# Performance work log

Hardware: AMD Instinct MI355X
Metric: run time of the kernel (lower is better)

The kernel has to match this reference:

```python
import jax, jax.numpy as jnp
import numpy as np

N_NODES = 100000
N_EDGES = 3200000
D_IN = 16
D_OUT = 32


def setup_inputs() -> dict:
    key = jax.random.key(0)
    ks = jax.random.split(key, 8)
    x = jax.random.normal(ks[0], (N_NODES, D_IN), dtype=jnp.float32)
    edge_index = jax.random.randint(ks[1], (2, N_EDGES), 0, N_NODES, dtype=jnp.int64)
    s = 1.0 / np.sqrt(D_IN)
    # mlp1: Linear(16,16) -> ReLU -> Linear(16,16)
    w1 = jax.random.uniform(ks[2], (D_IN, D_IN), jnp.float32, -s, s)
    b1 = jax.random.uniform(ks[3], (D_IN,), jnp.float32, -s, s)
    w2 = jax.random.uniform(ks[4], (D_IN, D_IN), jnp.float32, -s, s)
    b2 = jax.random.uniform(ks[5], (D_IN,), jnp.float32, -s, s)
    # SAGEConv(16,32): lin_l (neighbors, with bias), lin_r (root, no bias)
    wl = jax.random.uniform(ks[6], (D_IN, D_OUT), jnp.float32, -s, s)
    bl = jnp.zeros((D_OUT,), jnp.float32)
    wr = jax.random.uniform(ks[7], (D_IN, D_OUT), jnp.float32, -s, s)
    return {"x": x, "edge_index": edge_index, "w1": w1, "b1": b1,
            "w2": w2, "b2": b2, "wl": wl, "bl": bl, "wr": wr}


def reference(x, edge_index, w1, b1, w2, b2, wl, bl, wr):
    # MLP: Linear -> ReLU -> Linear
    h = jax.nn.relu(x @ w1 + b1) @ w2 + b2  # [N, 16]
    src, dst = edge_index[0], edge_index[1]
    # mean aggregation of neighbor (source) features at destination nodes
    msg = h[src]  # [E, 16]
    summed = jax.ops.segment_sum(msg, dst, num_segments=N_NODES)  # [N, 16]
    cnt = jax.ops.segment_sum(jnp.ones((msg.shape[0],), h.dtype), dst,
                              num_segments=N_NODES)
    mean = summed / jnp.maximum(cnt, 1.0)[:, None]
    # SAGEConv: lin_l(aggr) + lin_r(root)
    out = mean @ wl + bl + h @ wr  # [N, 32]
    return out
```

## Files before the change

kernel.cpp:

```cpp
#include <hip/hip_runtime.h>

#define D_IN_C 16
#define D_OUT_C 32
#define NB_LOG 6
#define NB (1 << NB_LOG)
#define NB_MASK (NB - 1)
#define MAXBUCK 1600
#define EPB 12800

__global__ __launch_bounds__(256) void mlp_kernel(
    const float* __restrict__ x,
    const float* __restrict__ w1, const float* __restrict__ b1,
    const float* __restrict__ w2, const float* __restrict__ b2,
    float* __restrict__ h, float* __restrict__ summed, int* __restrict__ cnt,
    int* __restrict__ gcount, int nbuck, int n_nodes) {
  __shared__ float sw1[256];
  __shared__ float sw2[256];
  __shared__ float sb1[16];
  __shared__ float sb2[16];
  int t = threadIdx.x;
  sw1[t] = w1[t];
  sw2[t] = w2[t];
  if (t < 16) { sb1[t] = b1[t]; sb2[t] = b2[t]; }
  __syncthreads();

  int n = blockIdx.x * blockDim.x + t;

  if (gcount && n < nbuck) gcount[n] = 0;
  if (n >= n_nodes) return;

  float xi[16];
  const float4* xr = (const float4*)(x + (size_t)n * 16);
  float4 v0 = xr[0], v1 = xr[1], v2 = xr[2], v3 = xr[3];
  xi[0]=v0.x; xi[1]=v0.y; xi[2]=v0.z; xi[3]=v0.w;
  xi[4]=v1.x; xi[5]=v1.y; xi[6]=v1.z; xi[7]=v1.w;
  xi[8]=v2.x; xi[9]=v2.y; xi[10]=v2.z; xi[11]=v2.w;
  xi[12]=v3.x; xi[13]=v3.y; xi[14]=v3.z; xi[15]=v3.w;

  float t1[16];
#pragma unroll
  for (int j = 0; j < 16; ++j) {
    float acc = sb1[j];
#pragma unroll
    for (int k = 0; k < 16; ++k) acc += xi[k] * sw1[k * 16 + j];
    t1[j] = fmaxf(acc, 0.0f);
  }
  float hh[16];
#pragma unroll
  for (int j = 0; j < 16; ++j) {
    float acc = sb2[j];
#pragma unroll
    for (int k = 0; k < 16; ++k) acc += t1[k] * sw2[k * 16 + j];
    hh[j] = acc;
  }

  float4* hw = (float4*)(h + (size_t)n * 16);
  hw[0] = make_float4(hh[0], hh[1], hh[2], hh[3]);
  hw[1] = make_float4(hh[4], hh[5], hh[6], hh[7]);
  hw[2] = make_float4(hh[8], hh[9], hh[10], hh[11]);
  hw[3] = make_float4(hh[12], hh[13], hh[14], hh[15]);

  if (cnt) cnt[n] = 0;
  if (summed) {
    float4* sz = (float4*)(summed + (size_t)n * 16);
    float4 z = make_float4(0.f, 0.f, 0.f, 0.f);
    sz[0] = z; sz[1] = z; sz[2] = z; sz[3] = z;
  }
}

__global__ __launch_bounds__(1024) void hist_kernel(
    const int* __restrict__ dst, int* __restrict__ gcount,
    int nbuck, int n_edges) {
  __shared__ int lcnt[MAXBUCK];
  int t = threadIdx.x;
  for (int i = t; i < MAXBUCK; i += 1024) lcnt[i] = 0;
  __syncthreads();
  int e0 = blockIdx.x * EPB;
  int e1 = e0 + EPB; if (e1 > n_edges) e1 = n_edges;
  for (int e = e0 + t; e < e1; e += 1024)
    atomicAdd(&lcnt[dst[e] >> NB_LOG], 1);
  __syncthreads();
  for (int b = t; b < nbuck; b += 1024) {
    int c = lcnt[b];
    if (c) atomicAdd(&gcount[b], c);
  }
}

__global__ __launch_bounds__(256) void scan_kernel(
    const int* __restrict__ gcount, int* __restrict__ base,
    int* __restrict__ cursor, int nbuck) {
  __shared__ int ps[256];
  int t = threadIdx.x;
  int per = (nbuck + 255) / 256;
  int beg = t * per;
  int end = beg + per; if (end > nbuck) end = nbuck;
  int sum = 0;
  for (int i = beg; i < end; ++i) sum += gcount[i];
  ps[t] = sum;
  __syncthreads();
#pragma unroll
  for (int off = 1; off < 256; off <<= 1) {
    int add = (t >= off) ? ps[t - off] : 0;
    __syncthreads();
    ps[t] += add;
    __syncthreads();
  }
  int run = ps[t] - sum;
  for (int i = beg; i < end; ++i) {
    base[i] = run;
    cursor[i] = run;
    run += gcount[i];
  }
  if (t == 255) base[nbuck] = ps[255];
}

__global__ __launch_bounds__(1024) void bin_kernel(
    const int* __restrict__ src, const int* __restrict__ dst,
    int* __restrict__ cursor, unsigned int* __restrict__ ebuf,
    int nbuck, int n_edges) {
  __shared__ int lcnt[MAXBUCK];
  __shared__ int lspan[MAXBUCK];
  int t = threadIdx.x;
  for (int i = t; i < MAXBUCK; i += 1024) lcnt[i] = 0;
  __syncthreads();
  int e0 = blockIdx.x * EPB;
  int e1 = e0 + EPB; if (e1 > n_edges) e1 = n_edges;
  for (int e = e0 + t; e < e1; e += 1024)
    atomicAdd(&lcnt[dst[e] >> NB_LOG], 1);
  __syncthreads();
  for (int b = t; b < nbuck; b += 1024) {
    int c = lcnt[b];
    lspan[b] = c ? atomicAdd(&cursor[b], c) : 0;
    lcnt[b] = 0;
  }
  __syncthreads();
  for (int e = e0 + t; e < e1; e += 1024) {
    int d = dst[e];
    int b = d >> NB_LOG;
    int r = atomicAdd(&lcnt[b], 1);
    ebuf[lspan[b] + r] =
        ((unsigned int)src[e] << NB_LOG) | (unsigned int)(d & NB_MASK);
  }
}

__global__ __launch_bounds__(256) void agg_out_kernel(
    const float* __restrict__ h, const unsigned int* __restrict__ ebuf,
    const int* __restrict__ base,
    const float* __restrict__ wl, const float* __restrict__ bl,
    const float* __restrict__ wr, float* __restrict__ out, int n_nodes) {
  __shared__ float ssum[NB * 16];
  __shared__ int   scnt[NB];
  __shared__ float stg[4 * 8 * 64];
  __shared__ float swl[512];
  __shared__ float swr[512];
  __shared__ float sbl[32];

  int t = threadIdx.x;
  int b = blockIdx.x;

  for (int i = t; i < 512; i += 256) { swl[i] = wl[i]; swr[i] = wr[i]; }
  if (t < 32) sbl[t] = bl[t];
#pragma unroll
  for (int i = t; i < NB * 16; i += 256) ssum[i] = 0.0f;
  if (t < NB) scnt[t] = 0;
  __syncthreads();

  int beg = base[b];
  int end = base[b + 1];

  int wid  = t >> 6;
  int lane = t & 63;
  int cl   = lane >> 4;
  int k    = lane & 15;

  const char* hb = (const char*)h;
  float* stgw = &stg[wid * 512];

  for (int pb = beg + wid * 32; pb < end; pb += 128) {
    unsigned int e[8];
#pragma unroll
    for (int u = 0; u < 8; ++u) {
      int idx = pb + 4 * u + cl;
      int cidx = idx < end ? idx : end - 1;
      e[u] = ebuf[cidx];
    }
#pragma unroll
    for (int u = 0; u < 8; ++u) {
      const void* gp = (const void*)(hb + ((e[u] & ~63u) + (unsigned)(k << 2)));
      __builtin_amdgcn_global_load_lds(
          (const __attribute__((address_space(1))) void*)gp,
          (__attribute__((address_space(3))) void*)&stgw[u * 64], 4, 0, 0);
    }
    asm volatile("s_waitcnt vmcnt(0)" ::: "memory");
#pragma unroll
    for (int u = 0; u < 8; ++u) {
      int idx = pb + 4 * u + cl;
      if (idx < end) {
        float v = stgw[u * 64 + lane];
        int dl = (int)(e[u] & NB_MASK);
        atomicAdd(&ssum[dl * 16 + k], v);
        if (k == 0) atomicAdd(&scnt[dl], 1);
      }
    }
  }
  __syncthreads();

  int j = t & 31;
  for (int nl = t >> 5; nl < NB; nl += 8) {
    int n = b * NB + nl;
    if (n >= n_nodes) break;
    float inv = 1.0f / fmaxf((float)scnt[nl], 1.0f);
    float acc = sbl[j];
    const float* hr = h + (size_t)n * 16;
#pragma unroll
    for (int kk = 0; kk < 16; ++kk) {
      float mv = ssum[nl * 16 + kk] * inv;
      acc += mv * swl[kk * 32 + j] + hr[kk] * swr[kk * 32 + j];
    }
    out[(size_t)n * 32 + j] = acc;
  }
}

__global__ __launch_bounds__(256) void scatter_kernel(
    const int* __restrict__ src, const int* __restrict__ dst,
    const float* __restrict__ h, float* __restrict__ summed,
    int* __restrict__ cnt, long long n_edges) {
  long long tid = (long long)blockIdx.x * blockDim.x + threadIdx.x;
  long long e = tid >> 4;
  int k = (int)(tid & 15);
  if (e >= n_edges) return;
  int s = src[e];
  int d = dst[e];
  float val = h[(size_t)s * 16 + k];
  atomicAdd(&summed[(size_t)d * 16 + k], val);
  if (k == 0) atomicAdd(&cnt[d], 1);
}

__global__ __launch_bounds__(256) void out_kernel(
    const float* __restrict__ h, const float* __restrict__ summed,
    const int* __restrict__ cnt,
    const float* __restrict__ wl, const float* __restrict__ bl,
    const float* __restrict__ wr, float* __restrict__ out, int n_nodes) {
  __shared__ float swl[512];
  __shared__ float swr[512];
  __shared__ float sbl[32];
  int t = threadIdx.x;
  for (int i = t; i < 512; i += 256) { swl[i] = wl[i]; swr[i] = wr[i]; }
  if (t < 32) sbl[t] = bl[t];
  __syncthreads();

  int gid = blockIdx.x * 256 + t;
  int n = gid >> 5;
  int j = gid & 31;
  if (n >= n_nodes) return;

  float inv = 1.0f / fmaxf((float)cnt[n], 1.0f);
  const float* hr = h + (size_t)n * 16;
  const float* sr = summed + (size_t)n * 16;
  float acc = sbl[j];
#pragma unroll
  for (int k = 0; k < 16; ++k) {
    acc += sr[k] * inv * swl[k * 32 + j] + hr[k] * swr[k * 32 + j];
  }
  out[(size_t)n * 32 + j] = acc;
}

extern "C" void kernel_launch(void* const* d_in, const int* in_sizes, int n_in,
                              void* d_out, int out_size, void* d_ws, size_t ws_size,
                              hipStream_t stream) {
  const float* x  = (const float*)d_in[0];
  const int* eidx = (const int*)d_in[1];
  const float* w1 = (const float*)d_in[2];
  const float* b1 = (const float*)d_in[3];
  const float* w2 = (const float*)d_in[4];
  const float* b2 = (const float*)d_in[5];
  const float* wl = (const float*)d_in[6];
  const float* bl = (const float*)d_in[7];
  const float* wr = (const float*)d_in[8];
  float* out = (float*)d_out;

  const int n_nodes = in_sizes[0] / D_IN_C;
  const long long n_edges = (long long)in_sizes[1] / 2;
  const int* src = eidx;
  const int* dst = eidx + n_edges;

  const int node_blocks = (n_nodes + 255) / 256;
  const int nbuck = (n_nodes + NB - 1) / NB;
  const int epb_blocks = (int)((n_edges + EPB - 1) / EPB);

  float*        h      = (float*)d_ws;
  int*          gcount = (int*)(h + (size_t)n_nodes * 16);
  int*          cursor = gcount + nbuck;
  int*          base   = cursor + nbuck;
  unsigned int* ebuf   = (unsigned int*)(base + nbuck + 1);

  size_t need = ((size_t)n_nodes * 16 + 3ull * nbuck + 1 + (size_t)n_edges) * 4;

  if (ws_size >= need && nbuck <= MAXBUCK) {
    mlp_kernel<<<node_blocks, 256, 0, stream>>>(
        x, w1, b1, w2, b2, h, nullptr, nullptr, gcount, nbuck, n_nodes);
    hist_kernel<<<epb_blocks, 1024, 0, stream>>>(dst, gcount, nbuck, (int)n_edges);
    scan_kernel<<<1, 256, 0, stream>>>(gcount, base, cursor, nbuck);
    bin_kernel<<<epb_blocks, 1024, 0, stream>>>(src, dst, cursor, ebuf,
                                                nbuck, (int)n_edges);
    agg_out_kernel<<<nbuck, 256, 0, stream>>>(h, ebuf, base, wl, bl, wr, out,
                                              n_nodes);
  } else {
    float* summed = h + (size_t)n_nodes * 16;
    int*   fcnt   = (int*)(summed + (size_t)n_nodes * 16);
    mlp_kernel<<<node_blocks, 256, 0, stream>>>(
        x, w1, b1, w2, b2, h, summed, fcnt, nullptr, 0, n_nodes);
    {
      long long total = n_edges * 16;
      int blocks = (int)((total + 255) / 256);
      scatter_kernel<<<blocks, 256, 0, stream>>>(src, dst, h, summed, fcnt, n_edges);
    }
    {
      long long total = (long long)n_nodes * 32;
      int blocks = (int)((total + 255) / 256);
      out_kernel<<<blocks, 256, 0, stream>>>(h, summed, fcnt, wl, bl, wr, out, n_nodes);
    }
  }
}
```

Measured before the change: 481.1 us.

## Tile aggregation over fp16 source chunks staged in LDS with per-bucket edge sort

Stores h in fp16 and computes the root term (h@wr+bl) in the MLP kernel, writing it directly to out. Buckets grow to 256 destination nodes. Each block counting-sorts its edges by source chunk in LDS, then streams every 256-row fp16 chunk of h through a double-buffered LDS tile, so gathers read LDS instead of doing random global loads. Edges beyond the LDS capacity take a direct global-gather path. Risks include fp16 rounding of h, every block streaming all of h (nbuck×8KB each), and a serial scan done by one thread.

```diff
diff --git a/kernel.cpp b/kernel.cpp
--- a/kernel.cpp
+++ b/kernel.cpp
@@ -1,32 +1,33 @@
 #include <hip/hip_runtime.h>
+#include <hip/hip_fp16.h>
 
 #define D_IN_C 16
 #define D_OUT_C 32
-#define NB_LOG 6
-#define NB (1 << NB_LOG)
-#define NB_MASK (NB - 1)
-#define MAXBUCK 1600
+#define NBL 8
+#define NBx 256
+#define NBMASK 255
+#define MAXBUCK 512
 #define EPB 12800
-
-__global__ __launch_bounds__(256) void mlp_kernel(
+#define CAP 8704
+
+__global__ __launch_bounds__(256) void mlp16_kernel(
     const float* __restrict__ x,
     const float* __restrict__ w1, const float* __restrict__ b1,
     const float* __restrict__ w2, const float* __restrict__ b2,
-    float* __restrict__ h, float* __restrict__ summed, int* __restrict__ cnt,
+    const float* __restrict__ wr, const float* __restrict__ bl,
+    __half* __restrict__ h16, float* __restrict__ out,
     int* __restrict__ gcount, int nbuck, int n_nodes) {
-  __shared__ float sw1[256];
-  __shared__ float sw2[256];
-  __shared__ float sb1[16];
-  __shared__ float sb2[16];
-  int t = threadIdx.x;
-  sw1[t] = w1[t];
-  sw2[t] = w2[t];
+  __shared__ float sw1[256], sw2[256], swr[512];
+  __shared__ float sb1[16], sb2[16], sbl[32];
+  int t = threadIdx.x;
+  sw1[t] = w1[t]; sw2[t] = w2[t];
+  swr[t] = wr[t]; swr[t + 256] = wr[t + 256];
   if (t < 16) { sb1[t] = b1[t]; sb2[t] = b2[t]; }
-  __syncthreads();
-
-  int n = blockIdx.x * blockDim.x + t;
-
-  if (gcount && n < nbuck) gcount[n] = 0;
+  if (t < 32) sbl[t] = bl[t];
+  __syncthreads();
+
+  int n = blockIdx.x * 256 + t;
+  if (n < nbuck) gcount[n] = 0;
   if (n >= n_nodes) return;
 
   float xi[16];
@@ -42,7 +43,7 @@
   for (int j = 0; j < 16; ++j) {
     float acc = sb1[j];
 #pragma unroll
-    for (int k = 0; k < 16; ++k) acc += xi[k] * sw1[k * 16 + j];
+    for (int kk = 0; kk < 16; ++kk) acc += xi[kk] * sw1[kk * 16 + j];
     t1[j] = fmaxf(acc, 0.0f);
   }
   float hh[16];
@@ -50,22 +51,34 @@
   for (int j = 0; j < 16; ++j) {
     float acc = sb2[j];
 #pragma unroll
-    for (int k = 0; k < 16; ++k) acc += t1[k] * sw2[k * 16 + j];
+    for (int kk = 0; kk < 16; ++kk) acc += t1[kk] * sw2[kk * 16 + j];
     hh[j] = acc;
   }
 
-  float4* hw = (float4*)(h + (size_t)n * 16);
-  hw[0] = make_float4(hh[0], hh[1], hh[2], hh[3]);
-  hw[1] = make_float4(hh[4], hh[5], hh[6], hh[7]);
-  hw[2] = make_float4(hh[8], hh[9], hh[10], hh[11]);
-  hw[3] = make_float4(hh[12], hh[13], hh[14], hh[15]);
-
-  if (cnt) cnt[n] = 0;
-  if (summed) {
-    float4* sz = (float4*)(summed + (size_t)n * 16);
-    float4 z = make_float4(0.f, 0.f, 0.f, 0.f);
-    sz[0] = z; sz[1] = z; sz[2] = z; sz[3] = z;
-  }
+  unsigned int pk[8];
+#pragma unroll
+  for (int j = 0; j < 8; ++j) {
+    unsigned lo = __half_as_ushort(__float2half(hh[2 * j]));
+    unsigned hi = __half_as_ushort(__float2half(hh[2 * j + 1]));
+    pk[j] = lo | (hi << 16);
+  }
+  uint4* hw = (uint4*)(h16 + (size_t)n * 16);
+  hw[0] = make_uint4(pk[0], pk[1], pk[2], pk[3]);
+  hw[1] = make_uint4(pk[4], pk[5], pk[6], pk[7]);
+
+  float r[32];
+#pragma unroll
+  for (int j = 0; j < 32; ++j) r[j] = sbl[j];
+#pragma unroll
+  for (int kk = 0; kk < 16; ++kk) {
+    float hv = hh[kk];
+#pragma unroll
+    for (int j = 0; j < 32; ++j) r[j] += hv * swr[kk * 32 + j];
+  }
+  float4* ow = (float4*)(out + (size_t)n * 32);
+#pragma unroll
+  for (int q = 0; q < 8; ++q)
+    ow[q] = make_float4(r[4 * q], r[4 * q + 1], r[4 * q + 2], r[4 * q + 3]);
 }
 
 __global__ __launch_bounds__(1024) void hist_kernel(
@@ -78,7 +91,7 @@
   int e0 = blockIdx.x * EPB;
   int e1 = e0 + EPB; if (e1 > n_edges) e1 = n_edges;
   for (int e = e0 + t; e < e1; e += 1024)
-    atomicAdd(&lcnt[dst[e] >> NB_LOG], 1);
+    atomicAdd(&lcnt[dst[e] >> NBL], 1);
   __syncthreads();
   for (int b = t; b < nbuck; b += 1024) {
     int c = lcnt[b];
@@ -126,7 +139,7 @@
   int e0 = blockIdx.x * EPB;
   int e1 = e0 + EPB; if (e1 > n_edges) e1 = n_edges;
   for (int e = e0 + t; e < e1; e += 1024)
-    atomicAdd(&lcnt[dst[e] >> NB_LOG], 1);
+    atomicAdd(&lcnt[dst[e] >> NBL], 1);
   __syncthreads();
   for (int b = t; b < nbuck; b += 1024) {
     int c = lcnt[b];
@@ -136,89 +149,184 @@
   __syncthreads();
   for (int e = e0 + t; e < e1; e += 1024) {
     int d = dst[e];
-    int b = d >> NB_LOG;
+    int b = d >> NBL;
     int r = atomicAdd(&lcnt[b], 1);
     ebuf[lspan[b] + r] =
-        ((unsigned int)src[e] << NB_LOG) | (unsigned int)(d & NB_MASK);
-  }
-}
-
-__global__ __launch_bounds__(256) void agg_out_kernel(
-    const float* __restrict__ h, const unsigned int* __restrict__ ebuf,
-    const int* __restrict__ base,
-    const float* __restrict__ wl, const float* __restrict__ bl,
-    const float* __restrict__ wr, float* __restrict__ out, int n_nodes) {
-  __shared__ float ssum[NB * 16];
-  __shared__ int   scnt[NB];
-  __shared__ float stg[4 * 8 * 64];
+        ((unsigned int)src[e] << NBL) | (unsigned int)(d & NBMASK);
+  }
+}
+
+__global__ __launch_bounds__(256) void agg_tiled_kernel(
+    const __half* __restrict__ h16, const unsigned int* __restrict__ ebuf,
+    const int* __restrict__ base, const float* __restrict__ wl,
+    float* __restrict__ out, int nbuck, int n_nodes) {
+  __shared__ unsigned short entS[CAP];
+  __shared__ __align__(16) __half bufs[2 * 4096];
+  __shared__ float ssum[NBx * 16];
+  __shared__ int   scnt[NBx];
+  __shared__ int   ccnt[MAXBUCK];
+  __shared__ int   coff[MAXBUCK + 1];
   __shared__ float swl[512];
-  __shared__ float swr[512];
-  __shared__ float sbl[32];
 
   int t = threadIdx.x;
   int b = blockIdx.x;
-
-  for (int i = t; i < 512; i += 256) { swl[i] = wl[i]; swr[i] = wr[i]; }
-  if (t < 32) sbl[t] = bl[t];
-#pragma unroll
-  for (int i = t; i < NB * 16; i += 256) ssum[i] = 0.0f;
-  if (t < NB) scnt[t] = 0;
+  int nch = nbuck;
+
+  swl[t] = wl[t]; swl[t + 256] = wl[t + 256];
+#pragma unroll
+  for (int i = t; i < NBx * 16; i += 256) ssum[i] = 0.0f;
+  if (t < NBx) scnt[t] = 0;
+  for (int i = t; i < MAXBUCK; i += 256) ccnt[i] = 0;
   __syncthreads();
 
   int beg = base[b];
   int end = base[b + 1];
-
-  int wid  = t >> 6;
-  int lane = t & 63;
-  int cl   = lane >> 4;
-  int k    = lane & 15;
-
-  const char* hb = (const char*)h;
-  float* stgw = &stg[wid * 512];
-
-  for (int pb = beg + wid * 32; pb < end; pb += 128) {
-    unsigned int e[8];
-#pragma unroll
-    for (int u = 0; u < 8; ++u) {
-      int idx = pb + 4 * u + cl;
-      int cidx = idx < end ? idx : end - 1;
-      e[u] = ebuf[cidx];
-    }
-#pragma unroll
-    for (int u = 0; u < 8; ++u) {
-      const void* gp = (const void*)(hb + ((e[u] & ~63u) + (unsigned)(k << 2)));
+  int ne = end - beg; if (ne > CAP) ne = CAP;
+
+  for (int i = t; i < ne; i += 256)
+    atomicAdd(&ccnt[ebuf[beg + i] >> 16], 1);
+  __syncthreads();
+  if (t == 0) {
+    int run = 0;
+    for (int c = 0; c < nch; ++c) {
+      int cc = ccnt[c];
+      coff[c] = run;
+      ccnt[c] = run;
+      run += cc;
+    }
+    coff[nch] = run;
+  }
+  __syncthreads();
+  for (int i = t; i < ne; i += 256) {
+    unsigned int ee = ebuf[beg + i];
+    int c = (int)(ee >> 16);
+    int r = atomicAdd(&ccnt[c], 1);
+    entS[r] = (unsigned short)(ee & 0xFFFFu);
+  }
+  __syncthreads();
+
+  int g = t >> 4;
+  int k = t & 15;
+
+  for (int p = beg + CAP + g; p < end; p += 16) {
+    unsigned int ee = ebuf[p];
+    unsigned int s = ee >> NBL;
+    int dl = (int)(ee & NBMASK);
+    float v = __half2float(h16[(size_t)s * 16 + k]);
+    atomicAdd(&ssum[dl * 16 + k], v);
+    if (k == 0) atomicAdd(&scnt[dl], 1);
+  }
+
+  const char* hb = (const char*)h16;
+  int wlane = t >> 6;
+  {
+    unsigned cbase = 0u;
+#pragma unroll
+    for (int i = 0; i < 2; ++i) {
+      const void* gp = (const void*)(hb + cbase + i * 4096 + t * 16);
+      char* lp = ((char*)bufs) + i * 4096 + wlane * 1024;
       __builtin_amdgcn_global_load_lds(
           (const __attribute__((address_space(1))) void*)gp,
-          (__attribute__((address_space(3))) void*)&stgw[u * 64], 4, 0, 0);
+          (__attribute__((address_space(3))) void*)lp, 16, 0, 0);
+    }
+  }
+  asm volatile("s_waitcnt vmcnt(0)" ::: "memory");
+  __syncthreads();
+
+  for (int c = 0; c < nch; ++c) {
+    if (c + 1 < nch) {
+      unsigned cbase = (unsigned)(c + 1) * (NBx * 32);
+      int bsel = (c + 1) & 1;
+#pragma unroll
+      for (int i = 0; i < 2; ++i) {
+        const void* gp = (const void*)(hb + cbase + i * 4096 + t * 16);
+        char* lp = ((char*)bufs) + bsel * 8192 + i * 4096 + wlane * 1024;
+        __builtin_amdgcn_global_load_lds(
+            (const __attribute__((address_space(1))) void*)gp,
+            (__attribute__((address_space(3))) void*)lp, 16, 0, 0);
+      }
+    }
+    const __half* hbuf = bufs + (c & 1) * 4096;
+    int cb = coff[c], ce = coff[c + 1];
+    for (int i = cb + g; i < ce; i += 16) {
+      unsigned short e2 = entS[i];
+      int sl = e2 >> 8;
+      int dl = e2 & 255;
+      float v = __half2float(hbuf[sl * 16 + k]);
+      atomicAdd(&ssum[dl * 16 + k], v);
+      if (k == 0) atomicAdd(&scnt[dl], 1);
     }
     asm volatile("s_waitcnt vmcnt(0)" ::: "memory");
-#pragma unroll
-    for (int u = 0; u < 8; ++u) {
-      int idx = pb + 4 * u + cl;
-      if (idx < end) {
-        float v = stgw[u * 64 + lane];
-        int dl = (int)(e[u] & NB_MASK);
-        atomicAdd(&ssum[dl * 16 + k], v);
-        if (k == 0) atomicAdd(&scnt[dl], 1);
-      }
-    }
-  }
-  __syncthreads();
+    __syncthreads();
+  }
 
   int j = t & 31;
-  for (int nl = t >> 5; nl < NB; nl += 8) {
-    int n = b * NB + nl;
+  for (int nl = t >> 5; nl < NBx; nl += 8) {
+    int n = b * NBx + nl;
     if (n >= n_nodes) break;
     float inv = 1.0f / fmaxf((float)scnt[nl], 1.0f);
-    float acc = sbl[j];
-    const float* hr = h + (size_t)n * 16;
-#pragma unroll
-    for (int kk = 0; kk < 16; ++kk) {
-      float mv = ssum[nl * 16 + kk] * inv;
-      acc += mv * swl[kk * 32 + j] + hr[kk] * swr[kk * 32 + j];
-    }
-    out[(size_t)n * 32 + j] = acc;
-  }
+    float acc = 0.0f;
+#pragma unroll
+    for (int kk = 0; kk < 16; ++kk)
+      acc += ssum[nl * 16 + kk] * inv * swl[kk * 32 + j];
+    out[(size_t)n * 32 + j] += acc;
+  }
+}
+
+__global__ __launch_bounds__(256) void mlp_kernel(
+    const float* __restrict__ x,
+    const float* __restrict__ w1, const float* __restrict__ b1,
+    const float* __restrict__ w2, const float* __restrict__ b2,
+    float* __restrict__ h, float* __restrict__ summed, int* __restrict__ cnt,
+    int n_nodes) {
+  __shared__ float sw1[256];
+  __shared__ float sw2[256];
+  __shared__ float sb1[16];
+  __shared__ float sb2[16];
+  int t = threadIdx.x;
+  sw1[t] = w1[t];
+  sw2[t] = w2[t];
+  if (t < 16) { sb1[t] = b1[t]; sb2[t] = b2[t]; }
+  __syncthreads();
+
+  int n = blockIdx.x * blockDim.x + t;
+  if (n >= n_nodes) return;
+
+  float xi[16];
+  const float4* xr = (const float4*)(x + (size_t)n * 16);
+  float4 v0 = xr[0], v1 = xr[1], v2 = xr[2], v3 = xr[3];
+  xi[0]=v0.x; xi[1]=v0.y; xi[2]=v0.z; xi[3]=v0.w;
+  xi[4]=v1.x; xi[5]=v1.y; xi[6]=v1.z; xi[7]=v1.w;
+  xi[8]=v2.x; xi[9]=v2.y; xi[10]=v2.z; xi[11]=v2.w;
+  xi[12]=v3.x; xi[13]=v3.y; xi[14]=v3.z; xi[15]=v3.w;
+
+  float t1[16];
+#pragma unroll
+  for (int j = 0; j < 16; ++j) {
+    float acc = sb1[j];
+#pragma unroll
+    for (int kk = 0; kk < 16; ++kk) acc += xi[kk] * sw1[kk * 16 + j];
+    t1[j] = fmaxf(acc, 0.0f);
+  }
+  float hh[16];
+#pragma unroll
+  for (int j = 0; j < 16; ++j) {
+    float acc = sb2[j];
+#pragma unroll
+    for (int kk = 0; kk < 16; ++kk) acc += t1[kk] * sw2[kk * 16 + j];
+    hh[j] = acc;
+  }
+
+  float4* hw = (float4*)(h + (size_t)n * 16);
+  hw[0] = make_float4(hh[0], hh[1], hh[2], hh[3]);
+  hw[1] = make_float4(hh[4], hh[5], hh[6], hh[7]);
+  hw[2] = make_float4(hh[8], hh[9], hh[10], hh[11]);
+  hw[3] = make_float4(hh[12], hh[13], hh[14], hh[15]);
+
+  cnt[n] = 0;
+  float4* sz = (float4*)(summed + (size_t)n * 16);
+  float4 z = make_float4(0.f, 0.f, 0.f, 0.f);
+  sz[0] = z; sz[1] = z; sz[2] = z; sz[3] = z;
 }
 
 __global__ __launch_bounds__(256) void scatter_kernel(
@@ -259,8 +367,8 @@
   const float* sr = summed + (size_t)n * 16;
   float acc = sbl[j];
 #pragma unroll
-  for (int k = 0; k < 16; ++k) {
-    acc += sr[k] * inv * swl[k * 32 + j] + hr[k] * swr[k * 32 + j];
+  for (int kk = 0; kk < 16; ++kk) {
+    acc += sr[kk] * inv * swl[kk * 32 + j] + hr[kk] * swr[kk * 32 + j];
   }
   out[(size_t)n * 32 + j] = acc;
 }
@@ -285,40 +393,46 @@
   const int* dst = eidx + n_edges;
 
   const int node_blocks = (n_nodes + 255) / 256;
-  const int nbuck = (n_nodes + NB - 1) / NB;
+  const int nbuck = (n_nodes + NBx - 1) / NBx;
+  const int padrows = nbuck * NBx;
   const int epb_blocks = (int)((n_edges + EPB - 1) / EPB);
 
-  float*        h      = (float*)d_ws;
-  int*          gcount = (int*)(h + (size_t)n_nodes * 16);
+  __half*       h16    = (__half*)d_ws;
+  int*          gcount = (int*)((char*)d_ws + (size_t)padrows * 32);
   int*          cursor = gcount + nbuck;
-  int*          base   = cursor + nbuck;
-  unsigned int* ebuf   = (unsigned int*)(base + nbuck + 1);
-
-  size_t need = ((size_t)n_nodes * 16 + 3ull * nbuck + 1 + (size_t)n_edges) * 4;
+  int*          basep  = cursor + nbuck;
+  unsigned int* ebuf   = (unsigned int*)(basep + nbuck + 1);
+
+  size_t need = (size_t)padrows * 32 + (3ull * nbuck + 1) * 4
+              + (size_t)n_edges * 4;
 
   if (ws_size >= need && nbuck <= MAXBUCK) {
-    mlp_kernel<<<node_blocks, 256, 0, stream>>>(
-        x, w1, b1, w2, b2, h, nullptr, nullptr, gcount, nbuck, n_nodes);
-    hist_kernel<<<epb_blocks, 1024, 0, stream>>>(dst, gcount, nbuck, (int)n_edges);
-    scan_kernel<<<1, 256, 0, stream>>>(gcount, base, cursor, nbuck);
+    mlp16_kernel<<<node_blocks, 256, 0, stream>>>(
+        x, w1, b1, w2, b2, wr, bl, h16, out, gcount, nbuck, n_nodes);
+    hist_kernel<<<epb_blocks, 1024, 0, stream>>>(dst, gcount, nbuck,
+                                                 (int)n_edges);
+    scan_kernel<<<1, 256, 0, stream>>>(gcount, basep, cursor, nbuck);
     bin_kernel<<<epb_blocks, 1024, 0, stream>>>(src, dst, cursor, ebuf,
                                                 nbuck, (int)n_edges);
-    agg_out_kernel<<<nbuck, 256, 0, stream>>>(h, ebuf, base, wl, bl, wr, out,
-                                              n_nodes);
+    agg_tiled_kernel<<<nbuck, 256, 0, stream>>>(h16, ebuf, basep, wl, out,
+                                                nbuck, n_nodes);
   } else {
+    float* h      = (float*)d_ws;
     float* summed = h + (size_t)n_nodes * 16;
     int*   fcnt   = (int*)(summed + (size_t)n_nodes * 16);
     mlp_kernel<<<node_blocks, 256, 0, stream>>>(
-        x, w1, b1, w2, b2, h, summed, fcnt, nullptr, 0, n_nodes);
+        x, w1, b1, w2, b2, h, summed, fcnt, n_nodes);
     {
       long long total = n_edges * 16;
       int blocks = (int)((total + 255) / 256);
-      scatter_kernel<<<blocks, 256, 0, stream>>>(src, dst, h, summed, fcnt, n_edges);
+      scatter_kernel<<<blocks, 256, 0, stream>>>(src, dst, h, summed, fcnt,
+                                                 n_edges);
     }
     {
       long long total = (long long)n_nodes * 32;
       int blocks = (int)((total + 255) / 256);
-      out_kernel<<<blocks, 256, 0, stream>>>(h, summed, fcnt, wl, bl, wr, out, n_nodes);
-    }
-  }
-}
+      out_kernel<<<blocks, 256, 0, stream>>>(h, summed, fcnt, wl, bl, wr,
+                                             out, n_nodes);
+    }
+  }
+}
```

Measured after the change: 622.8 us. 29.5% more time.
